# Kernel tuning notes

Hardware: AMD Instinct MI355X
Metric: run time of the kernel (lower is better)

The kernel has to match this reference:

```python
import jax, jax.numpy as jnp
import numpy as np

NUM_LAYERS = 2
VOCAB = 32000
IN_FEAT = 256          # embedding dim is IN_FEAT-1, +1 for cue scalar
HIDDEN = 256
ATN = 64               # hardcoded atn_feature_size in GraphConvolution
CLASSES = 2
B, N = 8, 2048


def setup_inputs() -> dict:
    key = jax.random.key(0)
    ks = jax.random.split(key, 12)
    x = jax.random.randint(ks[0], (B, N), 0, VOCAB, dtype=jnp.int32)
    cue = jax.random.randint(ks[1], (B, N), 0, 2, dtype=jnp.int32)
    adj = (jax.random.uniform(ks[2], (B, N, N)) < 0.01).astype(jnp.float32)
    s = 1.0 / np.sqrt(HIDDEN)
    emb_table = jax.random.normal(ks[3], (VOCAB, IN_FEAT - 1), jnp.float32) * 0.02
    Wh = jax.random.uniform(ks[4], (IN_FEAT, HIDDEN), jnp.float32, -s, s)
    bh = jax.random.uniform(ks[5], (HIDDEN,), jnp.float32, -s, s)
    Wq = jax.random.uniform(ks[6], (HIDDEN, ATN), jnp.float32, -s, s)
    Wk = jax.random.uniform(ks[7], (HIDDEN, ATN), jnp.float32, -s, s)
    Wv = jax.random.uniform(ks[8], (HIDDEN, HIDDEN), jnp.float32, -s, s)
    gcb = jax.random.uniform(ks[9], (HIDDEN,), jnp.float32, -s, s)
    Wc = jax.random.uniform(ks[10], (HIDDEN, CLASSES), jnp.float32, -s, s)
    bc = jax.random.uniform(ks[11], (CLASSES,), jnp.float32, -s, s)
    return {"x": x, "cue": cue, "adj": adj, "emb_table": emb_table,
            "Wh": Wh, "bh": bh, "Wq": Wq, "Wk": Wk, "Wv": Wv,
            "gcb": gcb, "Wc": Wc, "bc": bc}


def graph_attention_layer(h, adj, Wq, Wk, Wv, gcb):
    # h: [B,N,H]; adj: [B,N,N] binary. Per node i: softmax over neighbors j of
    # (Wk h_j) . (Wq h_i), weighted sum of Wv h_j. Zero-degree nodes get 0 (pre-bias).
    q = jnp.einsum('bnh,ha->bna', h, Wq)        # [B,N,A]
    k = jnp.einsum('bnh,ha->bna', h, Wk)        # [B,N,A]
    v = jnp.einsum('bnh,hg->bng', h, Wv)        # [B,N,H]
    logits = jnp.einsum('bia,bja->bij', q, k)   # [B,N,N]
    mask = adj > 0
    attn = jax.nn.softmax(jnp.where(mask, logits, -1e9), axis=-1)
    out = jnp.einsum('bij,bjh->bih', attn, v)   # [B,N,H]
    has_nbr = jnp.any(mask, axis=-1, keepdims=True)  # [B,N,1]
    return jnp.where(has_nbr, out, 0.0) + gcb


def reference(x, cue, adj, emb_table, Wh, bh, Wq, Wk, Wv, gcb, Wc, bc):
    emb = emb_table[x]                                   # [B,N,IN_FEAT-1]
    feats = jnp.concatenate([emb, cue.astype(jnp.float32)[..., None]], axis=-1)
    h = jax.nn.relu(jnp.einsum('bnf,fh->bnh', feats, Wh) + bh)
    for _ in range(NUM_LAYERS):
        h = jax.nn.sigmoid(graph_attention_layer(h, adj, Wq, Wk, Wv, gcb))
    logits = jnp.einsum('bnh,hc->bnc', h, Wc) + bc
    return jax.nn.softmax(logits, axis=-1)
```

## Files before the change

### kernel.cpp

```cpp
#include <hip/hip_runtime.h>
#include <hip/hip_bf16.h>


#define NB 8
#define NN 2048
#define ROWS (NB * NN)
#define MAXD 64

typedef float f4 __attribute__((ext_vector_type(4)));
typedef short bf8 __attribute__((ext_vector_type(8)));
typedef unsigned short u16;
typedef u16 us4 __attribute__((ext_vector_type(4)));
typedef u16 us8 __attribute__((ext_vector_type(8)));

__device__ __forceinline__ float sigmoidf_(float x) { return 1.f / (1.f + __expf(-x)); }
__device__ __forceinline__ u16 f2bf(float f) {
    unsigned u = __float_as_uint(f);
    u += 0x7fffu + ((u >> 16) & 1u);
    return (u16)(u >> 16);
}
__device__ __forceinline__ float bf2f(u16 h) {
    return __uint_as_float(((unsigned)h) << 16);
}

#define PACK_BLKS 96
#define EMB_BLKS 512

__global__ __launch_bounds__(256) void k_fused_front(
        const int* __restrict__ x, const int* __restrict__ cue,
        const float* __restrict__ adj, const float* __restrict__ emb,
        const float* __restrict__ Wh, const float* __restrict__ bh,
        const float* __restrict__ Wq, const float* __restrict__ Wk,
        const float* __restrict__ Wv,
        u16* __restrict__ hB, u16* __restrict__ Wpt,
        int* __restrict__ deg, int* __restrict__ nbr) {
    __shared__ float As[32 * 64];
    __shared__ float Ws[32 * 128];
    int bid = blockIdx.x;
    int t = threadIdx.x;

    if (bid < PACK_BLKS) {
        int idxp = bid * 256 + t;
#pragma unroll
        for (int r = 0; r < 4; ++r) {
            int i = idxp + r * PACK_BLKS * 256;
            int c = i >> 8, f = i & 255;
            float v;
            if (c < 64)       v = Wq[f * 64 + c];
            else if (c < 128) v = Wk[f * 64 + (c - 64)];
            else              v = Wv[f * 256 + (c - 128)];
            Wpt[i] = f2bf(v);
        }
        return;
    }

    if (bid < PACK_BLKS + EMB_BLKS) {
        int eb = bid - PACK_BLKS;
        int rt = eb >> 1, ct = eb & 1;
        int row0 = rt * 64, col0 = ct * 128;
        int sm = t & 63, skg = t >> 6;
        int swc = (t & 31) * 4, swk = t >> 5;
        int tx = t & 15, ty = t >> 4;
        int xr = x[row0 + sm];
        float cv = (float)cue[row0 + sm];
        const float* er = emb + (size_t)xr * 255;

        float acc[4][8];
#pragma unroll
        for (int i = 0; i < 4; ++i)
#pragma unroll
            for (int j = 0; j < 8; ++j) acc[i][j] = 0.f;

        for (int kc = 0; kc < 256; kc += 32) {
            int kb = skg * 8;
#pragma unroll
            for (int u = 0; u < 8; ++u) {
                int f = kc + kb + u;
                As[(kb + u) * 64 + sm] = (f < 255) ? er[f] : cv;
            }
#pragma unroll
            for (int r = 0; r < 4; ++r) {
                int kk = swk + r * 8;
                f4 w = *(const f4*)(Wh + (size_t)(kc + kk) * 256 + col0 + swc);
                *(f4*)&Ws[kk * 128 + swc] = w;
            }
            __syncthreads();
#pragma unroll
            for (int k = 0; k < 32; ++k) {
                f4 av = *(f4*)&As[k * 64 + ty * 4];
                f4 w0 = *(f4*)&Ws[k * 128 + tx * 8];
                f4 w1 = *(f4*)&Ws[k * 128 + tx * 8 + 4];
                float a[4] = {av.x, av.y, av.z, av.w};
                float w[8] = {w0.x, w0.y, w0.z, w0.w, w1.x, w1.y, w1.z, w1.w};
#pragma unroll
                for (int i = 0; i < 4; ++i)
#pragma unroll
                    for (int j = 0; j < 8; ++j) acc[i][j] += a[i] * w[j];
            }
            __syncthreads();
        }
        f4 b0 = *(const f4*)(bh + col0 + tx * 8);
        f4 b1 = *(const f4*)(bh + col0 + tx * 8 + 4);
        float bb[8] = {b0.x, b0.y, b0.z, b0.w, b1.x, b1.y, b1.z, b1.w};
#pragma unroll
        for (int i = 0; i < 4; ++i) {
            int row = row0 + ty * 4 + i;
            us8 o;
#pragma unroll
            for (int j = 0; j < 8; ++j) o[j] = f2bf(fmaxf(acc[i][j] + bb[j], 0.f));
            *(us8*)(hB + (size_t)row * 256 + col0 + tx * 8) = o;
        }
        return;
    }

    int row = bid - (PACK_BLKS + EMB_BLKS);
    const f4* ar4 = (const f4*)(adj + (size_t)row * NN);
    int* cnt = (int*)As;
    if (t == 0) *cnt = 0;
    __syncthreads();
    int* nr = nbr + (size_t)row * MAXD;
#pragma unroll
    for (int it = 0; it < 2; ++it) {
        int idx = it * 256 + t;
        f4 vv = __builtin_nontemporal_load(ar4 + idx);
        if (vv.x > 0.f) { int p = atomicAdd(cnt, 1); if (p < MAXD) nr[p] = idx * 4 + 0; }
        if (vv.y > 0.f) { int p = atomicAdd(cnt, 1); if (p < MAXD) nr[p] = idx * 4 + 1; }
        if (vv.z > 0.f) { int p = atomicAdd(cnt, 1); if (p < MAXD) nr[p] = idx * 4 + 2; }
        if (vv.w > 0.f) { int p = atomicAdd(cnt, 1); if (p < MAXD) nr[p] = idx * 4 + 3; }
    }
    __syncthreads();
    if (t == 0) deg[row] = (*cnt < MAXD) ? *cnt : MAXD;
}

__global__ __launch_bounds__(256) void k_qkv_mfma(const u16* __restrict__ hB,
                                                  const u16* __restrict__ Wpt,
                                                  float* __restrict__ q,
                                                  u16* __restrict__ kv) {
    __shared__ u16 As[64 * 40];
    __shared__ u16 Bs[128 * 40];
    int t = threadIdx.x;
    int col0 = blockIdx.x * 128, row0 = blockIdx.y * 64;
    int wave = t >> 6, lane = t & 63;
    int l16 = lane & 15, quad = lane >> 4;

    f4 acc[4][2];
#pragma unroll
    for (int i = 0; i < 4; ++i) { acc[i][0] = (f4){0,0,0,0}; acc[i][1] = (f4){0,0,0,0}; }

    int ar = t >> 2, ao = (t & 3) * 8;
    int bc = t >> 1, bo = (t & 1) * 16;

    for (int kc = 0; kc < 256; kc += 32) {
        us8 av  = *(const us8*)(hB  + (size_t)(row0 + ar) * 256 + kc + ao);
        us8 bv0 = *(const us8*)(Wpt + (size_t)(col0 + bc) * 256 + kc + bo);
        us8 bv1 = *(const us8*)(Wpt + (size_t)(col0 + bc) * 256 + kc + bo + 8);
        __syncthreads();
        *(us8*)&As[ar * 40 + ao] = av;
        *(us8*)&Bs[bc * 40 + bo] = bv0;
        *(us8*)&Bs[bc * 40 + bo + 8] = bv1;
        __syncthreads();
        bf8 afr[4], bfr[2];
#pragma unroll
        for (int mt = 0; mt < 4; ++mt)
            afr[mt] = *(bf8*)&As[(mt * 16 + l16) * 40 + quad * 8];
#pragma unroll
        for (int nt = 0; nt < 2; ++nt)
            bfr[nt] = *(bf8*)&Bs[((wave * 2 + nt) * 16 + l16) * 40 + quad * 8];
#pragma unroll
        for (int mt = 0; mt < 4; ++mt)
#pragma unroll
            for (int nt = 0; nt < 2; ++nt)
                acc[mt][nt] = __builtin_amdgcn_mfma_f32_16x16x32_bf16(
                    afr[mt], bfr[nt], acc[mt][nt], 0, 0, 0);
    }
#pragma unroll
    for (int mt = 0; mt < 4; ++mt)
#pragma unroll
        for (int nt = 0; nt < 2; ++nt) {
            int c = col0 + (wave * 2 + nt) * 16 + l16;
#pragma unroll
            for (int reg = 0; reg < 4; ++reg) {
                int r = row0 + mt * 16 + quad * 4 + reg;
                float val = acc[mt][nt][reg];
                if (c < 64) q[(size_t)r * 64 + c] = val;
                else        kv[(size_t)r * 320 + (c - 64)] = f2bf(val);
            }
        }
}

template <bool WRITE_OUT>
__global__ __launch_bounds__(256) void k_attn(const float* __restrict__ q,
                                              const u16* __restrict__ kv,
                                              const int* __restrict__ deg,
                                              const int* __restrict__ nbr,
                                              const float* __restrict__ gcb,
                                              const float* __restrict__ Wc,
                                              const float* __restrict__ bc,
                                              u16* __restrict__ hB,
                                              float* __restrict__ out) {
    int wave = threadIdx.x >> 6;
    int lane = threadIdx.x & 63;
    int row = blockIdx.x * 4 + wave;
    int d = deg[row];
    int l16 = lane & 15;
    f4 g4 = *(const f4*)(gcb + lane * 4);
    float h0, h1, h2, h3;
    if (d == 0) {
        h0 = sigmoidf_(g4.x); h1 = sigmoidf_(g4.y);
        h2 = sigmoidf_(g4.z); h3 = sigmoidf_(g4.w);
    } else {
        f4 q4 = *(const f4*)(q + (size_t)row * 64 + l16 * 4);
        const int* jl = nbr + (size_t)row * MAXD;
        int bbase = row & ~(NN - 1);
        float m = -1e30f, s = 0.f;
        f4 a = {0, 0, 0, 0};
        for (int e = 0; e < d; e += 4) {
            int idx = e + (lane >> 4);
            int jg = jl[idx < d ? idx : 0];
            const u16* kr = kv + (size_t)(bbase + jg) * 320;
            us4 kq = *(const us4*)(kr + l16 * 4);
            float p = q4.x * bf2f(kq.x) + q4.y * bf2f(kq.y)
                    + q4.z * bf2f(kq.z) + q4.w * bf2f(kq.w);
            p += __shfl_xor(p, 1); p += __shfl_xor(p, 2);
            p += __shfl_xor(p, 4); p += __shfl_xor(p, 8);
            if (idx >= d) p = -1e30f;
            float p0 = __shfl(p, 0),  p1 = __shfl(p, 16);
            float p2 = __shfl(p, 32), p3 = __shfl(p, 48);
            int j0 = __shfl(jg, 0),  j1 = __shfl(jg, 16);
            int j2 = __shfl(jg, 32), j3 = __shfl(jg, 48);
            float mx = fmaxf(fmaxf(p0, p1), fmaxf(p2, p3));
            float mn = fmaxf(m, mx);
            float scale = __expf(m - mn);
            float w0 = __expf(p0 - mn), w1 = __expf(p1 - mn);
            float w2 = __expf(p2 - mn), w3 = __expf(p3 - mn);
            s = s * scale + ((w0 + w1) + (w2 + w3));
            us4 u0 = *(const us4*)(kv + (size_t)(bbase + j0) * 320 + 64 + lane * 4);
            us4 u1 = *(const us4*)(kv + (size_t)(bbase + j1) * 320 + 64 + lane * 4);
            us4 u2 = *(const us4*)(kv + (size_t)(bbase + j2) * 320 + 64 + lane * 4);
            us4 u3 = *(const us4*)(kv + (size_t)(bbase + j3) * 320 + 64 + lane * 4);
            a.x = a.x * scale + w0 * bf2f(u0.x) + w1 * bf2f(u1.x) + w2 * bf2f(u2.x) + w3 * bf2f(u3.x);
            a.y = a.y * scale + w0 * bf2f(u0.y) + w1 * bf2f(u1.y) + w2 * bf2f(u2.y) + w3 * bf2f(u3.y);
            a.z = a.z * scale + w0 * bf2f(u0.z) + w1 * bf2f(u1.z) + w2 * bf2f(u2.z) + w3 * bf2f(u3.z);
            a.w = a.w * scale + w0 * bf2f(u0.w) + w1 * bf2f(u1.w) + w2 * bf2f(u2.w) + w3 * bf2f(u3.w);
            m = mn;
        }
        float inv = 1.f / s;
        h0 = sigmoidf_(a.x * inv + g4.x);
        h1 = sigmoidf_(a.y * inv + g4.y);
        h2 = sigmoidf_(a.z * inv + g4.z);
        h3 = sigmoidf_(a.w * inv + g4.w);
    }
    if (!WRITE_OUT) {
        us4 o;
        o.x = f2bf(h0); o.y = f2bf(h1); o.z = f2bf(h2); o.w = f2bf(h3);
        *(us4*)(hB + (size_t)row * 256 + lane * 4) = o;
    } else {
        f4 wc0 = *(const f4*)(Wc + lane * 8);
        f4 wc1 = *(const f4*)(Wc + lane * 8 + 4);
        float pa = h0 * wc0.x + h1 * wc0.z + h2 * wc1.x + h3 * wc1.z;
        float pb = h0 * wc0.y + h1 * wc0.w + h2 * wc1.y + h3 * wc1.w;
#pragma unroll
        for (int off = 32; off; off >>= 1) {
            pa += __shfl_xor(pa, off);
            pb += __shfl_xor(pb, off);
        }
        if (lane == 0) {
            float l0 = pa + bc[0], l1 = pb + bc[1];
            float mx = fmaxf(l0, l1);
            float e0 = __expf(l0 - mx), e1 = __expf(l1 - mx);
            float inv = 1.f / (e0 + e1);
            out[(size_t)row * 2 + 0] = e0 * inv;
            out[(size_t)row * 2 + 1] = e1 * inv;
        }
    }
}

extern "C" void kernel_launch(void* const* d_in, const int* in_sizes, int n_in,
                              void* d_out, int out_size, void* d_ws, size_t ws_size,
                              hipStream_t stream) {
    const int*   x    = (const int*)d_in[0];
    const int*   cue  = (const int*)d_in[1];
    const float* adj  = (const float*)d_in[2];
    const float* emb  = (const float*)d_in[3];
    const float* Wh   = (const float*)d_in[4];
    const float* bh   = (const float*)d_in[5];
    const float* Wq   = (const float*)d_in[6];
    const float* Wk   = (const float*)d_in[7];
    const float* Wv   = (const float*)d_in[8];
    const float* gcb  = (const float*)d_in[9];
    const float* Wc   = (const float*)d_in[10];
    const float* bc   = (const float*)d_in[11];
    float* out = (float*)d_out;

    char* w = (char*)d_ws;
    u16*   hB  = (u16*)w;                 w += (size_t)ROWS * 256 * 2;
    float* q   = (float*)w;               w += (size_t)ROWS * 64 * 4;
    u16*   kv  = (u16*)w;                 w += (size_t)ROWS * 320 * 2;
    u16*   Wpt = (u16*)w;                 w += (size_t)384 * 256 * 2;
    int*   deg = (int*)w;                 w += (size_t)ROWS * 4;
    int*   nbr = (int*)w;

    k_fused_front<<<PACK_BLKS + EMB_BLKS + ROWS, 256, 0, stream>>>(
        x, cue, adj, emb, Wh, bh, Wq, Wk, Wv, hB, Wpt, deg, nbr);
    k_qkv_mfma<<<dim3(3, ROWS / 64), 256, 0, stream>>>(hB, Wpt, q, kv);
    k_attn<false><<<ROWS / 4, 256, 0, stream>>>(q, kv, deg, nbr, gcb, Wc, bc, hB, out);
    k_qkv_mfma<<<dim3(3, ROWS / 64), 256, 0, stream>>>(hB, Wpt, q, kv);
    k_attn<true><<<ROWS / 4, 256, 0, stream>>>(q, kv, deg, nbr, gcb, Wc, bc, hB, out);
}
```

Baseline: 329.1 us.

## Prefetch neighbor keys and GEMM tiles, remap blocks across XCDs

The attention loop now loads the neighbor indices as a vector and prefetches the next group's key fragment while the current group is processed. Value loads are issued before the score reduction, and the broadcast shuffles are replaced with xor shuffles. The QKV GEMM register-prefetches the next k-chunk. Block indices in all three kernels are permuted so that neighbouring rows land on the same XCD for L2 locality. Neighbor list padding is zeroed so prefetches read valid indices, at the cost of more registers and extra index math.

```diff
diff --git a/kernel.cpp b/kernel.cpp
--- a/kernel.cpp
+++ b/kernel.cpp
@@ -12,6 +12,7 @@
 typedef unsigned short u16;
 typedef u16 us4 __attribute__((ext_vector_type(4)));
 typedef u16 us8 __attribute__((ext_vector_type(8)));
+typedef int i4 __attribute__((ext_vector_type(4)));
 
 __device__ __forceinline__ float sigmoidf_(float x) { return 1.f / (1.f + __expf(-x)); }
 __device__ __forceinline__ u16 f2bf(float f) {
@@ -55,8 +56,9 @@
     }
 
     if (bid < PACK_BLKS + EMB_BLKS) {
-        int eb = bid - PACK_BLKS;
-        int rt = eb >> 1, ct = eb & 1;
+        int rb2 = bid - PACK_BLKS;
+        int v2 = ((rb2 & 7) << 6) + (rb2 >> 3);
+        int rt = v2 >> 1, ct = v2 & 1;
         int row0 = rt * 64, col0 = ct * 128;
         int sm = t & 63, skg = t >> 6;
         int swc = (t & 31) * 4, swk = t >> 5;
@@ -113,7 +115,8 @@
         return;
     }
 
-    int row = bid - (PACK_BLKS + EMB_BLKS);
+    int rb = bid - (PACK_BLKS + EMB_BLKS);
+    int row = ((rb & 7) << 11) + (rb >> 3);
     const f4* ar4 = (const f4*)(adj + (size_t)row * NN);
     int* cnt = (int*)As;
     if (t == 0) *cnt = 0;
@@ -129,7 +132,9 @@
         if (vv.w > 0.f) { int p = atomicAdd(cnt, 1); if (p < MAXD) nr[p] = idx * 4 + 3; }
     }
     __syncthreads();
-    if (t == 0) deg[row] = (*cnt < MAXD) ? *cnt : MAXD;
+    int c = *cnt; if (c > MAXD) c = MAXD;
+    if (t == 0) deg[row] = c;
+    if (t < MAXD && t >= c) nr[t] = 0;
 }
 
 __global__ __launch_bounds__(256) void k_qkv_mfma(const u16* __restrict__ hB,
@@ -139,7 +144,9 @@
     __shared__ u16 As[64 * 40];
     __shared__ u16 Bs[128 * 40];
     int t = threadIdx.x;
-    int col0 = blockIdx.x * 128, row0 = blockIdx.y * 64;
+    int flat = blockIdx.x + blockIdx.y * 3;
+    int v = ((flat & 7) * 96) + (flat >> 3);
+    int col0 = (v % 3) * 128, row0 = (v / 3) * 64;
     int wave = t >> 6, lane = t & 63;
     int l16 = lane & 15, quad = lane >> 4;
 
@@ -149,16 +156,25 @@
 
     int ar = t >> 2, ao = (t & 3) * 8;
     int bc = t >> 1, bo = (t & 1) * 16;
-
+    const u16* aP = hB  + (size_t)(row0 + ar) * 256 + ao;
+    const u16* bP = Wpt + (size_t)(col0 + bc) * 256 + bo;
+
+    us8 av  = *(const us8*)(aP);
+    us8 bv0 = *(const us8*)(bP);
+    us8 bv1 = *(const us8*)(bP + 8);
+
+#pragma unroll
     for (int kc = 0; kc < 256; kc += 32) {
-        us8 av  = *(const us8*)(hB  + (size_t)(row0 + ar) * 256 + kc + ao);
-        us8 bv0 = *(const us8*)(Wpt + (size_t)(col0 + bc) * 256 + kc + bo);
-        us8 bv1 = *(const us8*)(Wpt + (size_t)(col0 + bc) * 256 + kc + bo + 8);
         __syncthreads();
         *(us8*)&As[ar * 40 + ao] = av;
         *(us8*)&Bs[bc * 40 + bo] = bv0;
         *(us8*)&Bs[bc * 40 + bo + 8] = bv1;
         __syncthreads();
+        if (kc + 32 < 256) {
+            av  = *(const us8*)(aP + kc + 32);
+            bv0 = *(const us8*)(bP + kc + 32);
+            bv1 = *(const us8*)(bP + kc + 40);
+        }
         bf8 afr[4], bfr[2];
 #pragma unroll
         for (int mt = 0; mt < 4; ++mt)
@@ -200,9 +216,12 @@
                                               float* __restrict__ out) {
     int wave = threadIdx.x >> 6;
     int lane = threadIdx.x & 63;
-    int row = blockIdx.x * 4 + wave;
+    int bid = blockIdx.x;
+    int vb = ((bid & 7) << 9) + (bid >> 3);
+    int row = vb * 4 + wave;
     int d = deg[row];
     int l16 = lane & 15;
+    int g = lane >> 4;
     f4 g4 = *(const f4*)(gcb + lane * 4);
     float h0, h1, h2, h3;
     if (d == 0) {
@@ -214,35 +233,41 @@
         int bbase = row & ~(NN - 1);
         float m = -1e30f, s = 0.f;
         f4 a = {0, 0, 0, 0};
+        i4 jj = *(const i4*)(jl);
+        int jg = (g == 0) ? jj.x : (g == 1) ? jj.y : (g == 2) ? jj.z : jj.w;
+        us4 kq = *(const us4*)(kv + (size_t)(bbase + jg) * 320 + l16 * 4);
         for (int e = 0; e < d; e += 4) {
-            int idx = e + (lane >> 4);
-            int jg = jl[idx < d ? idx : 0];
-            const u16* kr = kv + (size_t)(bbase + jg) * 320;
-            us4 kq = *(const us4*)(kr + l16 * 4);
+            int en = (e + 4 < d) ? (e + 4) : 0;
+            i4 jjn = *(const i4*)(jl + en);
+            int jgn = (g == 0) ? jjn.x : (g == 1) ? jjn.y : (g == 2) ? jjn.z : jjn.w;
+            us4 kqn = *(const us4*)(kv + (size_t)(bbase + jgn) * 320 + l16 * 4);
+            int ja = (g == 0) ? jj.y : (g == 1) ? jj.x : (g == 2) ? jj.w : jj.z;
+            int jb = (g == 0) ? jj.z : (g == 1) ? jj.w : (g == 2) ? jj.x : jj.y;
+            int jc = (g == 0) ? jj.w : (g == 1) ? jj.z : (g == 2) ? jj.y : jj.x;
+            us4 u0 = *(const us4*)(kv + (size_t)(bbase + jg) * 320 + 64 + lane * 4);
+            us4 u1 = *(const us4*)(kv + (size_t)(bbase + ja) * 320 + 64 + lane * 4);
+            us4 u2 = *(const us4*)(kv + (size_t)(bbase + jb) * 320 + 64 + lane * 4);
+            us4 u3 = *(const us4*)(kv + (size_t)(bbase + jc) * 320 + 64 + lane * 4);
             float p = q4.x * bf2f(kq.x) + q4.y * bf2f(kq.y)
                     + q4.z * bf2f(kq.z) + q4.w * bf2f(kq.w);
             p += __shfl_xor(p, 1); p += __shfl_xor(p, 2);
             p += __shfl_xor(p, 4); p += __shfl_xor(p, 8);
-            if (idx >= d) p = -1e30f;
-            float p0 = __shfl(p, 0),  p1 = __shfl(p, 16);
-            float p2 = __shfl(p, 32), p3 = __shfl(p, 48);
-            int j0 = __shfl(jg, 0),  j1 = __shfl(jg, 16);
-            int j2 = __shfl(jg, 32), j3 = __shfl(jg, 48);
-            float mx = fmaxf(fmaxf(p0, p1), fmaxf(p2, p3));
+            if (e + g >= d) p = -1e30f;
+            float pa = __shfl_xor(p, 16);
+            float pb = __shfl_xor(p, 32);
+            float pc = __shfl_xor(pa, 32);
+            float mx = fmaxf(fmaxf(p, pa), fmaxf(pb, pc));
             float mn = fmaxf(m, mx);
             float scale = __expf(m - mn);
-            float w0 = __expf(p0 - mn), w1 = __expf(p1 - mn);
-            float w2 = __expf(p2 - mn), w3 = __expf(p3 - mn);
+            float w0 = __expf(p - mn),  w1 = __expf(pa - mn);
+            float w2 = __expf(pb - mn), w3 = __expf(pc - mn);
             s = s * scale + ((w0 + w1) + (w2 + w3));
-            us4 u0 = *(const us4*)(kv + (size_t)(bbase + j0) * 320 + 64 + lane * 4);
-            us4 u1 = *(const us4*)(kv + (size_t)(bbase + j1) * 320 + 64 + lane * 4);
-            us4 u2 = *(const us4*)(kv + (size_t)(bbase + j2) * 320 + 64 + lane * 4);
-            us4 u3 = *(const us4*)(kv + (size_t)(bbase + j3) * 320 + 64 + lane * 4);
             a.x = a.x * scale + w0 * bf2f(u0.x) + w1 * bf2f(u1.x) + w2 * bf2f(u2.x) + w3 * bf2f(u3.x);
             a.y = a.y * scale + w0 * bf2f(u0.y) + w1 * bf2f(u1.y) + w2 * bf2f(u2.y) + w3 * bf2f(u3.y);
             a.z = a.z * scale + w0 * bf2f(u0.z) + w1 * bf2f(u1.z) + w2 * bf2f(u2.z) + w3 * bf2f(u3.z);
             a.w = a.w * scale + w0 * bf2f(u0.w) + w1 * bf2f(u1.w) + w2 * bf2f(u2.w) + w3 * bf2f(u3.w);
             m = mn;
+            jj = jjn; jg = jgn; kq = kqn;
         }
         float inv = 1.f / s;
         h0 = sigmoidf_(a.x * inv + g4.x);
```

Measured after the change: 328.1 us. Within noise of the previous version (-0.3%).
